# Performance work log

Measured on AMD Instinct MI355X. Metric: run time of the kernel, lower is better.

Reference implementation:

```python
import jax, jax.numpy as jnp
import numpy as np

D_MODEL = 1024
D_HIDDEN = 4096
N_EXPERTS = 8
B, S = 2, 2048


def setup_inputs() -> dict:
    key = jax.random.key(0)
    ks = jax.random.split(key, 4)
    sd = 1.0 / np.sqrt(D_MODEL)
    sh = 1.0 / np.sqrt(D_HIDDEN)
    return {
        "x": jax.random.normal(ks[0], (B, S, D_MODEL), dtype=jnp.float32),
        "Wg": jax.random.normal(ks[1], (D_MODEL, N_EXPERTS), dtype=jnp.float32) * sd,
        "bg": jnp.zeros((N_EXPERTS,), dtype=jnp.float32),
        "W1": jax.random.normal(ks[2], (N_EXPERTS, D_MODEL, D_HIDDEN), dtype=jnp.float32) * sd,
        "b1": jnp.zeros((N_EXPERTS, D_HIDDEN), dtype=jnp.float32),
        "W2": jax.random.normal(ks[3], (N_EXPERTS, D_HIDDEN, D_MODEL), dtype=jnp.float32) * sh,
        "b2": jnp.zeros((N_EXPERTS, D_MODEL), dtype=jnp.float32),
    }


def reference(x, Wg, bg, W1, b1, W2, b2):
    # Router: softmax is monotone, so argmax(softmax(logits)) == argmax(logits).
    logits = jnp.einsum("bsd,de->bse", x, Wg) + bg
    expert_idx = jnp.argmax(logits, axis=-1)  # [B, S]
    # Top-1 dispatch, expressed as compute-all-experts + per-token select
    # (jit-friendly; the torch loop masks/gathers per expert).
    h = jax.nn.gelu(jnp.einsum("bsd,edh->bseh", x, W1) + b1, approximate=False)
    y = jnp.einsum("bseh,ehd->bsed", h, W2) + b2  # [B, S, E, D]
    out = jnp.take_along_axis(y, expert_idx[:, :, None, None], axis=2)[:, :, 0, :]
    return out
```

## Files before the change

kernel.cpp:

```cpp
#include <hip/hip_runtime.h>
#include <hip/hip_bf16.h>
#include <math.h>

#define D_MODEL 1024
#define D_HIDDEN 4096
#define N_EXP 8
#define N_TOK 4096

typedef __attribute__((ext_vector_type(8))) __bf16 bf16x8_t;
typedef __attribute__((ext_vector_type(4))) float f32x4_t;

#define WS_BUCKET_OFF 256
#define WS_XB_OFF     ((size_t)1 << 18)
#define WS_H_OFF      (((size_t)1 << 18) + ((size_t)8 << 20))
#define WS_W1B_OFF    (((size_t)1 << 18) + ((size_t)40 << 20))
#define WS_W2B_OFF    (((size_t)1 << 18) + ((size_t)104 << 20))
#define WS_NEED       (((size_t)1 << 18) + ((size_t)168 << 20))

__device__ __forceinline__ void gload16(const void* g, void* l) {
    __builtin_amdgcn_global_load_lds(
        (__attribute__((address_space(1))) void*)(g),
        (__attribute__((address_space(3))) void*)(l),
        16, 0, 0);
}

template<int N> __device__ __forceinline__ void waitcnt_vm() {
    if constexpr (N >= 8)      asm volatile("s_waitcnt vmcnt(8)" ::: "memory");
    else if constexpr (N == 6) asm volatile("s_waitcnt vmcnt(6)" ::: "memory");
    else if constexpr (N == 4) asm volatile("s_waitcnt vmcnt(4)" ::: "memory");
    else                       asm volatile("s_waitcnt vmcnt(0)" ::: "memory");
}

__global__ __launch_bounds__(64) void init_counts(int* counts) {
    if (threadIdx.x < N_EXP) counts[threadIdx.x] = 0;
}

__global__ __launch_bounds__(256) void router_kernel(
    const float* __restrict__ x, const float* __restrict__ Wg,
    const float* __restrict__ bg, int* __restrict__ counts,
    int* __restrict__ bucket, __hip_bfloat16* __restrict__ xb)
{
    const int wid  = threadIdx.x >> 6;
    const int lane = threadIdx.x & 63;
    const int t    = blockIdx.x * 4 + wid;
    const float* xr = x + (size_t)t * D_MODEL;

    double acc[N_EXP];
#pragma unroll
    for (int e = 0; e < N_EXP; ++e) acc[e] = 0.0;

#pragma unroll
    for (int j = 0; j < D_MODEL / 64; ++j) {
        const int d = j * 64 + lane;
        const float xv = xr[d];
        xb[(size_t)t * D_MODEL + d] = __float2bfloat16(xv);
        const float4* wr = (const float4*)(Wg + (size_t)d * N_EXP);
        const float4 w0 = wr[0], w1 = wr[1];
        const double xd = (double)xv;
        acc[0] += xd * (double)w0.x; acc[1] += xd * (double)w0.y;
        acc[2] += xd * (double)w0.z; acc[3] += xd * (double)w0.w;
        acc[4] += xd * (double)w1.x; acc[5] += xd * (double)w1.y;
        acc[6] += xd * (double)w1.z; acc[7] += xd * (double)w1.w;
    }
#pragma unroll
    for (int e = 0; e < N_EXP; ++e) {
        double v = acc[e];
#pragma unroll
        for (int off = 32; off >= 1; off >>= 1) v += __shfl_xor(v, off, 64);
        acc[e] = v + (double)bg[e];
    }
    if (lane == 0) {
        int best = 0; double bv = acc[0];
#pragma unroll
        for (int e = 1; e < N_EXP; ++e)
            if (acc[e] > bv) { bv = acc[e]; best = e; }
        const int pos = atomicAdd(&counts[best], 1);
        bucket[best * N_TOK + pos] = t;
    }
}

template<int KT, int NT>
__global__ __launch_bounds__(256) void convert_w(
    const float* __restrict__ W, __hip_bfloat16* __restrict__ Wb)
{
    const int e  = blockIdx.z;
    const int k0 = blockIdx.y * 64;
    const int n0 = blockIdx.x * 64;
    const int tid = threadIdx.x;

    __shared__ __hip_bfloat16 Lt[64 * 68];

    const int q  = tid & 15;
    const int kb = tid >> 4;
    const float* src = W + (size_t)e * KT * NT + (size_t)(k0 + kb * 4) * NT + n0 + q * 4;
    float4 v0 = *(const float4*)(src);
    float4 v1 = *(const float4*)(src + (size_t)NT);
    float4 v2 = *(const float4*)(src + (size_t)2 * NT);
    float4 v3 = *(const float4*)(src + (size_t)3 * NT);
#pragma unroll
    for (int i = 0; i < 4; ++i) {
        union { __hip_bfloat16 hh[4]; unsigned long long u; } pk;
        pk.hh[0] = __float2bfloat16(((const float*)&v0)[i]);
        pk.hh[1] = __float2bfloat16(((const float*)&v1)[i]);
        pk.hh[2] = __float2bfloat16(((const float*)&v2)[i]);
        pk.hh[3] = __float2bfloat16(((const float*)&v3)[i]);
        *(unsigned long long*)((char*)Lt + (size_t)(q * 4 + i) * 136 + kb * 8) = pk.u;
    }
    __syncthreads();

    const int w    = tid >> 6;
    const int lane = tid & 63;
    const int nr   = w * 16 + (lane >> 2);
    const int half = lane & 3;
    const char* rp = (const char*)Lt + (size_t)nr * 136 + half * 32;
    const uint2 a0 = *(const uint2*)(rp);
    const uint2 a1 = *(const uint2*)(rp + 8);
    const uint2 b0 = *(const uint2*)(rp + 16);
    const uint2 b1 = *(const uint2*)(rp + 24);
    __hip_bfloat16* op = Wb + (size_t)e * NT * KT + (size_t)(n0 + nr) * KT + k0 + half * 16;
    *(uint4*)op       = make_uint4(a0.x, a0.y, a1.x, a1.y);
    *(uint4*)(op + 8) = make_uint4(b0.x, b0.y, b1.x, b1.y);
}

template<int K_TOT, int N_TOT, int BN, bool IS_FFN1>
__global__ __launch_bounds__(256) void ffn_gemm_bf16(
    const __hip_bfloat16* __restrict__ A,
    const __hip_bfloat16* __restrict__ Wb,
    const float* __restrict__ bias,
    const int* __restrict__ counts,
    const int* __restrict__ bucket,
    __hip_bfloat16* __restrict__ hout,
    float* __restrict__ yout)
{
    constexpr int NG  = BN / 32;
    constexpr int NBI = BN / 32;
    constexpr int NB  = N_TOT / BN;
    constexpr int MB  = N_TOK / 128;
    constexpr int NWG = NB * MB * N_EXP;
    constexpr int ASZ = 128 * 64 * 2;
    constexpr int BSZ = BN * 64 * 2;
    constexpr int NT  = K_TOT / 64;
    constexpr int L   = 4 + NBI;

    const int orig = blockIdx.x;
    const int wg   = (orig & 7) * (NWG >> 3) + (orig >> 3);
    const int e    = wg / (NB * MB);
    const int rem  = wg % (NB * MB);
    const int n0   = (rem / MB) * BN;
    const int m0   = (rem % MB) * 128;

    const int cnt = counts[e];
    if (m0 >= cnt) return;
    const int tid  = threadIdx.x;
    const int lane = tid & 63;
    const int wid  = tid >> 6;
    const int wm   = wid >> 1, wn = wid & 1;

    __shared__ __hip_bfloat16 As[2 * 128 * 64];
    __shared__ __hip_bfloat16 Bs[2 * BN * 64];
    __shared__ int s_tok[128];

    if (tid < 128) {
        int idx = m0 + tid;
        if (idx >= cnt) idx = cnt - 1;
        s_tok[tid] = bucket[e * N_TOK + idx];
    }
    __syncthreads();

    const __hip_bfloat16* gA[4]; char* lA[4];
#pragma unroll
    for (int i = 0; i < 4; ++i) {
        const int r = wid * 32 + i * 8 + (lane >> 3);
        gA[i] = A + (size_t)s_tok[r] * K_TOT + (((lane & 7) ^ (r & 7)) << 3);
        lA[i] = (char*)As + (size_t)(wid * 32 + i * 8) * 128;
    }
    const __hip_bfloat16* gB[NBI]; char* lB[NBI];
    const __hip_bfloat16* wbase = Wb + (size_t)e * N_TOT * K_TOT;
#pragma unroll
    for (int i = 0; i < NBI; ++i) {
        const int r = wid * (BN / 4) + i * 8 + (lane >> 3);
        gB[i] = wbase + (size_t)(n0 + r) * K_TOT + (((lane & 7) ^ (r & 7)) << 3);
        lB[i] = (char*)Bs + (size_t)(wid * (BN / 4) + i * 8) * 128;
    }

    f32x4_t acc[4][NG];
#pragma unroll
    for (int f = 0; f < 4; ++f)
#pragma unroll
        for (int g = 0; g < NG; ++g) acc[f][g] = (f32x4_t){0.f, 0.f, 0.f, 0.f};

#pragma unroll
    for (int i = 0; i < 4; ++i) gload16(gA[i], lA[i]);
#pragma unroll
    for (int i = 0; i < NBI; ++i) gload16(gB[i], lB[i]);
    waitcnt_vm<0>();
    __builtin_amdgcn_s_barrier();

    for (int t = 0; t < NT; ++t) {
        const int c = t & 1;
        if (t + 1 < NT) {
            const int k1 = (t + 1) * 64;
#pragma unroll
            for (int i = 0; i < 4; ++i) gload16(gA[i] + k1, lA[i] + (c ^ 1) * ASZ);
#pragma unroll
            for (int i = 0; i < NBI; ++i) gload16(gB[i] + k1, lB[i] + (c ^ 1) * BSZ);
            waitcnt_vm<L>();
        } else {
            waitcnt_vm<0>();
        }
        __builtin_amdgcn_s_barrier();
        __builtin_amdgcn_sched_barrier(0);

        const char* asb = (const char*)As + c * ASZ;
        const char* bsb = (const char*)Bs + c * BSZ;
#pragma unroll
        for (int kk = 0; kk < 2; ++kk) {
            uint4 af[4], bf[NG];
            const int ko = kk * 4 + (lane >> 4);
#pragma unroll
            for (int f = 0; f < 4; ++f) {
                const int r = wm * 64 + f * 16 + (lane & 15);
                af[f] = *(const uint4*)(asb + r * 128 + ((ko ^ (r & 7)) << 4));
            }
#pragma unroll
            for (int g = 0; g < NG; ++g) {
                const int n = wn * (BN / 2) + g * 16 + (lane & 15);
                bf[g] = *(const uint4*)(bsb + n * 128 + ((ko ^ (n & 7)) << 4));
            }
#pragma unroll
            for (int f = 0; f < 4; ++f)
#pragma unroll
                for (int g = 0; g < NG; ++g)
                    acc[f][g] = __builtin_amdgcn_mfma_f32_16x16x32_bf16(
                        __builtin_bit_cast(bf16x8_t, af[f]),
                        __builtin_bit_cast(bf16x8_t, bf[g]),
                        acc[f][g], 0, 0, 0);
        }
        __builtin_amdgcn_s_barrier();
    }

#pragma unroll
    for (int f = 0; f < 4; ++f) {
#pragma unroll
        for (int j = 0; j < 4; ++j) {
            const int rl = wm * 64 + f * 16 + (lane >> 4) * 4 + j;
            const bool ok = (m0 + rl) < cnt;
            const int tok = s_tok[rl];
#pragma unroll
            for (int g = 0; g < NG; ++g) {
                const int col = n0 + wn * (BN / 2) + g * 16 + (lane & 15);
                float v = acc[f][g][j] + bias[e * N_TOT + col];
                if (IS_FFN1) {
                    v = 0.5f * v * (1.0f + erff(v * 0.70710678118654752f));
                    if (ok) hout[(size_t)tok * N_TOT + col] = __float2bfloat16(v);
                } else {
                    if (ok) yout[(size_t)tok * N_TOT + col] = v;
                }
            }
        }
    }
}

template<int K_TOT, int N_TOT, bool IS_FFN1>
__global__ __launch_bounds__(256, 2) void ffn_gemm_f32(
    const __hip_bfloat16* __restrict__ A,
    const float* __restrict__ W,
    const float* __restrict__ bias,
    const int* __restrict__ counts,
    const int* __restrict__ bucket,
    __hip_bfloat16* __restrict__ hout,
    float* __restrict__ yout)
{
    const int e   = blockIdx.z;
    const int cnt = counts[e];
    const int m0  = blockIdx.y * 128;
    if (m0 >= cnt) return;
    const int n0   = blockIdx.x * 128;
    const int tid  = threadIdx.x;
    const int lane = tid & 63;
    const int wid  = tid >> 6;
    const int wm   = wid >> 1, wn = wid & 1;

    __shared__ __hip_bfloat16 As[128 * 64];
    __shared__ __hip_bfloat16 Bs[128 * 64];
    __shared__ int s_tok[128];

    if (tid < 128) {
        int idx = m0 + tid;
        if (idx >= cnt) idx = cnt - 1;
        s_tok[tid] = bucket[e * N_TOK + idx];
    }
    __syncthreads();

    const __hip_bfloat16* gA[4]; char* lA[4];
#pragma unroll
    for (int i = 0; i < 4; ++i) {
        const int r = wid * 32 + i * 8 + (lane >> 3);
        gA[i] = A + (size_t)s_tok[r] * K_TOT + (((lane & 7) ^ (r & 7)) << 3);
        lA[i] = (char*)As + (size_t)(wid * 32 + i * 8) * 128;
    }
    const int ko_t = lane & 7;
    const int nq   = wid * 8 + (lane >> 3);
    const float* wb = W + (size_t)e * K_TOT * N_TOT + (size_t)(ko_t * 8) * N_TOT + n0 + nq * 4;

    f32x4_t acc[4][4];
#pragma unroll
    for (int f = 0; f < 4; ++f)
#pragma unroll
        for (int g = 0; g < 4; ++g) acc[f][g] = (f32x4_t){0.f, 0.f, 0.f, 0.f};

    for (int k0 = 0; k0 < K_TOT; k0 += 64) {
#pragma unroll
        for (int i = 0; i < 4; ++i) gload16(gA[i] + k0, lA[i]);
        const float* wk = wb + (size_t)k0 * N_TOT;
        float4 v[8];
#pragma unroll
        for (int j = 0; j < 8; ++j) v[j] = *(const float4*)(wk + (size_t)j * N_TOT);
#pragma unroll
        for (int i = 0; i < 4; ++i) {
            const int n = nq * 4 + i;
            union { __hip_bfloat16 hh[8]; uint4 u; } pk;
#pragma unroll
            for (int j = 0; j < 8; ++j) pk.hh[j] = __float2bfloat16(((const float*)&v[j])[i]);
            *(uint4*)((char*)Bs + n * 128 + ((ko_t ^ (n & 7)) << 4)) = pk.u;
        }
        __syncthreads();

#pragma unroll
        for (int kk = 0; kk < 2; ++kk) {
            uint4 af[4], bf[4];
            const int ko = kk * 4 + (lane >> 4);
#pragma unroll
            for (int f = 0; f < 4; ++f) {
                const int r = wm * 64 + f * 16 + (lane & 15);
                af[f] = *(const uint4*)((const char*)As + r * 128 + ((ko ^ (r & 7)) << 4));
            }
#pragma unroll
            for (int g = 0; g < 4; ++g) {
                const int n = wn * 64 + g * 16 + (lane & 15);
                bf[g] = *(const uint4*)((const char*)Bs + n * 128 + ((ko ^ (n & 7)) << 4));
            }
#pragma unroll
            for (int f = 0; f < 4; ++f)
#pragma unroll
                for (int g = 0; g < 4; ++g)
                    acc[f][g] = __builtin_amdgcn_mfma_f32_16x16x32_bf16(
                        __builtin_bit_cast(bf16x8_t, af[f]),
                        __builtin_bit_cast(bf16x8_t, bf[g]),
                        acc[f][g], 0, 0, 0);
        }
        __syncthreads();
    }

#pragma unroll
    for (int f = 0; f < 4; ++f) {
#pragma unroll
        for (int j = 0; j < 4; ++j) {
            const int rl = wm * 64 + f * 16 + (lane >> 4) * 4 + j;
            const bool ok = (m0 + rl) < cnt;
            const int tok = s_tok[rl];
#pragma unroll
            for (int g = 0; g < 4; ++g) {
                const int col = n0 + wn * 64 + g * 16 + (lane & 15);
                float v = acc[f][g][j] + bias[e * N_TOT + col];
                if (IS_FFN1) {
                    v = 0.5f * v * (1.0f + erff(v * 0.70710678118654752f));
                    if (ok) hout[(size_t)tok * N_TOT + col] = __float2bfloat16(v);
                } else {
                    if (ok) yout[(size_t)tok * N_TOT + col] = v;
                }
            }
        }
    }
}

extern "C" void kernel_launch(void* const* d_in, const int* in_sizes, int n_in,
                              void* d_out, int out_size, void* d_ws, size_t ws_size,
                              hipStream_t stream) {
    const float* x  = (const float*)d_in[0];
    const float* Wg = (const float*)d_in[1];
    const float* bg = (const float*)d_in[2];
    const float* W1 = (const float*)d_in[3];
    const float* b1 = (const float*)d_in[4];
    const float* W2 = (const float*)d_in[5];
    const float* b2 = (const float*)d_in[6];
    float* out = (float*)d_out;

    char* ws = (char*)d_ws;
    int* counts = (int*)(ws);
    int* bucket = (int*)(ws + WS_BUCKET_OFF);
    __hip_bfloat16* xb  = (__hip_bfloat16*)(ws + WS_XB_OFF);
    __hip_bfloat16* h   = (__hip_bfloat16*)(ws + WS_H_OFF);
    __hip_bfloat16* w1b = (__hip_bfloat16*)(ws + WS_W1B_OFF);
    __hip_bfloat16* w2b = (__hip_bfloat16*)(ws + WS_W2B_OFF);

    init_counts<<<dim3(1), dim3(64), 0, stream>>>(counts);
    router_kernel<<<dim3(N_TOK / 4), dim3(256), 0, stream>>>(x, Wg, bg, counts, bucket, xb);

    if (ws_size >= WS_NEED) {
        convert_w<D_MODEL, D_HIDDEN><<<dim3(D_HIDDEN / 64, D_MODEL / 64, N_EXP), dim3(256), 0, stream>>>(W1, w1b);
        convert_w<D_HIDDEN, D_MODEL><<<dim3(D_MODEL / 64, D_HIDDEN / 64, N_EXP), dim3(256), 0, stream>>>(W2, w2b);
        ffn_gemm_bf16<D_MODEL, D_HIDDEN, 128, true>
            <<<dim3((D_HIDDEN / 128) * (N_TOK / 128) * N_EXP), dim3(256), 0, stream>>>(
                xb, w1b, b1, counts, bucket, h, nullptr);
        ffn_gemm_bf16<D_HIDDEN, D_MODEL, 64, false>
            <<<dim3((D_MODEL / 64) * (N_TOK / 128) * N_EXP), dim3(256), 0, stream>>>(
                h, w2b, b2, counts, bucket, nullptr, out);
    } else {
        ffn_gemm_f32<D_MODEL, D_HIDDEN, true>
            <<<dim3(D_HIDDEN / 128, N_TOK / 128, N_EXP), dim3(256), 0, stream>>>(
                xb, W1, b1, counts, bucket, h, nullptr);
        ffn_gemm_f32<D_HIDDEN, D_MODEL, false>
            <<<dim3(D_MODEL / 128, N_TOK / 128, N_EXP), dim3(256), 0, stream>>>(
                h, W2, b2, counts, bucket, nullptr, out);
    }
}
```

Baseline: 380.9 us.

## Pre-tile gathered activations and weights into contiguous swizzled chunks for GEMMs

Adds a prefix kernel and a gather kernel that copies each expert's routed tokens into contiguous, pre-swizzled 128x64 bf16 tiles, and rewrites weight conversion to emit the same tiled swizzled layout. The GEMMs then issue fully contiguous global-to-LDS loads with no per-row indirection, and FFN1 writes its hidden output directly in the tiled layout that FFN2 consumes. The aim is to remove scattered row gathers and strided loads from the main loops. In exchange it adds an extra gather pass over x, two more launches and a larger workspace requirement.

```diff
diff --git a/kernel.cpp b/kernel.cpp
--- a/kernel.cpp
+++ b/kernel.cpp
@@ -10,12 +10,15 @@
 typedef __attribute__((ext_vector_type(8))) __bf16 bf16x8_t;
 typedef __attribute__((ext_vector_type(4))) float f32x4_t;
 
+#define WS_PREFIX_OFF 128
 #define WS_BUCKET_OFF 256
 #define WS_XB_OFF     ((size_t)1 << 18)
-#define WS_H_OFF      (((size_t)1 << 18) + ((size_t)8 << 20))
-#define WS_W1B_OFF    (((size_t)1 << 18) + ((size_t)40 << 20))
-#define WS_W2B_OFF    (((size_t)1 << 18) + ((size_t)104 << 20))
-#define WS_NEED       (((size_t)1 << 18) + ((size_t)168 << 20))
+#define WS_HT_OFF     (((size_t)1 << 18) + ((size_t)8 << 20))
+#define WS_W1T_OFF    (((size_t)1 << 18) + ((size_t)50 << 20))
+#define WS_W2T_OFF    (((size_t)1 << 18) + ((size_t)114 << 20))
+#define WS_AE_OFF     (((size_t)1 << 18) + ((size_t)178 << 20))
+#define WS_NEED       (((size_t)1 << 18) + ((size_t)189 << 20))
+#define WS_NEED_FB    (((size_t)1 << 18) + ((size_t)40 << 20))
 
 __device__ __forceinline__ void gload16(const void* g, void* l) {
     __builtin_amdgcn_global_load_lds(
@@ -33,6 +36,14 @@
 
 __global__ __launch_bounds__(64) void init_counts(int* counts) {
     if (threadIdx.x < N_EXP) counts[threadIdx.x] = 0;
+}
+
+__global__ __launch_bounds__(64) void prefix_kernel(const int* counts, int* prefix) {
+    if (threadIdx.x == 0) {
+        int s = 0;
+#pragma unroll
+        for (int e = 0; e < N_EXP; ++e) { prefix[e] = s; s += (counts[e] + 127) >> 7; }
+    }
 }
 
 __global__ __launch_bounds__(256) void router_kernel(
@@ -79,55 +90,110 @@
     }
 }
 
-template<int KT, int NT>
-__global__ __launch_bounds__(256) void convert_w(
-    const float* __restrict__ W, __hip_bfloat16* __restrict__ Wb)
-{
-    const int e  = blockIdx.z;
-    const int k0 = blockIdx.y * 64;
-    const int n0 = blockIdx.x * 64;
+__global__ __launch_bounds__(256) void convert_w1(
+    const float* __restrict__ W, __hip_bfloat16* __restrict__ Wt)
+{
+    const int nblk = blockIdx.x, kc = blockIdx.y, e = blockIdx.z;
+    const int k0 = kc * 64, n0 = nblk * 128;
     const int tid = threadIdx.x;
-
-    __shared__ __hip_bfloat16 Lt[64 * 68];
-
-    const int q  = tid & 15;
-    const int kb = tid >> 4;
-    const float* src = W + (size_t)e * KT * NT + (size_t)(k0 + kb * 4) * NT + n0 + q * 4;
-    float4 v0 = *(const float4*)(src);
-    float4 v1 = *(const float4*)(src + (size_t)NT);
-    float4 v2 = *(const float4*)(src + (size_t)2 * NT);
-    float4 v3 = *(const float4*)(src + (size_t)3 * NT);
-#pragma unroll
-    for (int i = 0; i < 4; ++i) {
-        union { __hip_bfloat16 hh[4]; unsigned long long u; } pk;
-        pk.hh[0] = __float2bfloat16(((const float*)&v0)[i]);
-        pk.hh[1] = __float2bfloat16(((const float*)&v1)[i]);
-        pk.hh[2] = __float2bfloat16(((const float*)&v2)[i]);
-        pk.hh[3] = __float2bfloat16(((const float*)&v3)[i]);
-        *(unsigned long long*)((char*)Lt + (size_t)(q * 4 + i) * 136 + kb * 8) = pk.u;
+    __shared__ __hip_bfloat16 Lt[128 * 72];
+
+    const int kr = tid >> 2;
+    const int cq = tid & 3;
+    const float* src = W + (size_t)e * D_MODEL * D_HIDDEN + (size_t)(k0 + kr) * D_HIDDEN + n0 + cq * 32;
+#pragma unroll
+    for (int f = 0; f < 8; ++f) {
+        const float4 v = *(const float4*)(src + f * 4);
+#pragma unroll
+        for (int j = 0; j < 4; ++j) {
+            const int n = cq * 32 + f * 4 + j;
+            *(__hip_bfloat16*)((char*)Lt + (size_t)n * 144 + kr * 2) = __float2bfloat16(((const float*)&v)[j]);
+        }
     }
     __syncthreads();
 
-    const int w    = tid >> 6;
-    const int lane = tid & 63;
-    const int nr   = w * 16 + (lane >> 2);
-    const int half = lane & 3;
-    const char* rp = (const char*)Lt + (size_t)nr * 136 + half * 32;
-    const uint2 a0 = *(const uint2*)(rp);
-    const uint2 a1 = *(const uint2*)(rp + 8);
-    const uint2 b0 = *(const uint2*)(rp + 16);
-    const uint2 b1 = *(const uint2*)(rp + 24);
-    __hip_bfloat16* op = Wb + (size_t)e * NT * KT + (size_t)(n0 + nr) * KT + k0 + half * 16;
-    *(uint4*)op       = make_uint4(a0.x, a0.y, a1.x, a1.y);
-    *(uint4*)(op + 8) = make_uint4(b0.x, b0.y, b1.x, b1.y);
+    char* outc = (char*)Wt + (((size_t)e * 32 + nblk) * 16 + kc) * 16384;
+    const int n = tid >> 1, half = tid & 1;
+#pragma unroll
+    for (int s = 0; s < 4; ++s) {
+        const int slot = half * 4 + s;
+        const int ko = slot ^ (n & 7);
+        const uint4 v = *(const uint4*)((const char*)Lt + (size_t)n * 144 + ko * 16);
+        *(uint4*)(outc + (size_t)n * 128 + slot * 16) = v;
+    }
+}
+
+__global__ __launch_bounds__(256) void convert_w2(
+    const float* __restrict__ W, __hip_bfloat16* __restrict__ Wt)
+{
+    const int nblk = blockIdx.x, kc = blockIdx.y, e = blockIdx.z;
+    const int k0 = kc * 64, n0 = nblk * 64;
+    const int tid = threadIdx.x;
+    __shared__ __hip_bfloat16 Lt[64 * 72];
+
+    const int kr = tid >> 2;
+    const int cq = tid & 3;
+    const float* src = W + (size_t)e * D_HIDDEN * D_MODEL + (size_t)(k0 + kr) * D_MODEL + n0 + cq * 16;
+#pragma unroll
+    for (int f = 0; f < 4; ++f) {
+        const float4 v = *(const float4*)(src + f * 4);
+#pragma unroll
+        for (int j = 0; j < 4; ++j) {
+            const int n = cq * 16 + f * 4 + j;
+            *(__hip_bfloat16*)((char*)Lt + (size_t)n * 144 + kr * 2) = __float2bfloat16(((const float*)&v)[j]);
+        }
+    }
+    __syncthreads();
+
+    char* outc = (char*)Wt + (((size_t)e * 16 + nblk) * 64 + kc) * 8192;
+    const int n = tid >> 2, q = tid & 3;
+#pragma unroll
+    for (int s = 0; s < 2; ++s) {
+        const int slot = q * 2 + s;
+        const int ko = slot ^ (n & 7);
+        const uint4 v = *(const uint4*)((const char*)Lt + (size_t)n * 144 + ko * 16);
+        *(uint4*)(outc + (size_t)n * 128 + slot * 16) = v;
+    }
+}
+
+__global__ __launch_bounds__(256) void gather_a(
+    const float* __restrict__ x, const int* __restrict__ counts,
+    const int* __restrict__ prefix, const int* __restrict__ bucket,
+    __hip_bfloat16* __restrict__ Ae)
+{
+    const int mblk = blockIdx.x, kc = blockIdx.y, e = blockIdx.z;
+    const int cnt = counts[e];
+    if (mblk * 128 >= cnt) return;
+    const int mbg = prefix[e] + mblk;
+    const int tid = threadIdx.x;
+    const int m = tid >> 1, half = tid & 1;
+    int idx = mblk * 128 + m;
+    if (idx >= cnt) idx = cnt - 1;
+    const int tok = bucket[e * N_TOK + idx];
+    const float* src = x + (size_t)tok * D_MODEL + kc * 64 + half * 32;
+    char* dst = (char*)Ae + ((size_t)mbg * 16 + kc) * 16384 + (size_t)m * 128;
+#pragma unroll
+    for (int s = 0; s < 4; ++s) {
+        const float4 a = *(const float4*)(src + s * 8);
+        const float4 b = *(const float4*)(src + s * 8 + 4);
+        union { __hip_bfloat16 hh[8]; uint4 u; } pk;
+#pragma unroll
+        for (int j = 0; j < 4; ++j) {
+            pk.hh[j]     = __float2bfloat16(((const float*)&a)[j]);
+            pk.hh[j + 4] = __float2bfloat16(((const float*)&b)[j]);
+        }
+        const int ko = half * 4 + s;
+        *(uint4*)(dst + ((ko ^ (m & 7)) << 4)) = pk.u;
+    }
 }
 
 template<int K_TOT, int N_TOT, int BN, bool IS_FFN1>
-__global__ __launch_bounds__(256) void ffn_gemm_bf16(
-    const __hip_bfloat16* __restrict__ A,
-    const __hip_bfloat16* __restrict__ Wb,
+__global__ __launch_bounds__(256) void ffn_gemm_t(
+    const __hip_bfloat16* __restrict__ At,
+    const __hip_bfloat16* __restrict__ Wt,
     const float* __restrict__ bias,
     const int* __restrict__ counts,
+    const int* __restrict__ prefix,
     const int* __restrict__ bucket,
     __hip_bfloat16* __restrict__ hout,
     float* __restrict__ yout)
@@ -137,51 +203,44 @@
     constexpr int NB  = N_TOT / BN;
     constexpr int MB  = N_TOK / 128;
     constexpr int NWG = NB * MB * N_EXP;
-    constexpr int ASZ = 128 * 64 * 2;
-    constexpr int BSZ = BN * 64 * 2;
-    constexpr int NT  = K_TOT / 64;
+    constexpr int KC  = K_TOT / 64;
+    constexpr int ACH = 16384;
+    constexpr int BCH = BN * 128;
+    constexpr int ASZ = 16384;
+    constexpr int BSZ = BN * 128;
     constexpr int L   = 4 + NBI;
 
     const int orig = blockIdx.x;
     const int wg   = (orig & 7) * (NWG >> 3) + (orig >> 3);
     const int e    = wg / (NB * MB);
     const int rem  = wg % (NB * MB);
-    const int n0   = (rem / MB) * BN;
-    const int m0   = (rem % MB) * 128;
-
-    const int cnt = counts[e];
+    const int nblk = rem / MB;
+    const int mblk = rem % MB;
+    const int cnt  = counts[e];
+    const int m0   = mblk * 128;
     if (m0 >= cnt) return;
+    const int mbg  = prefix[e] + mblk;
+    const int n0   = nblk * BN;
+
     const int tid  = threadIdx.x;
     const int lane = tid & 63;
     const int wid  = tid >> 6;
     const int wm   = wid >> 1, wn = wid & 1;
 
-    __shared__ __hip_bfloat16 As[2 * 128 * 64];
-    __shared__ __hip_bfloat16 Bs[2 * BN * 64];
+    __shared__ char As[2 * ASZ];
+    __shared__ char Bs[2 * BSZ];
     __shared__ int s_tok[128];
 
-    if (tid < 128) {
+    if (!IS_FFN1 && tid < 128) {
         int idx = m0 + tid;
         if (idx >= cnt) idx = cnt - 1;
         s_tok[tid] = bucket[e * N_TOK + idx];
     }
-    __syncthreads();
-
-    const __hip_bfloat16* gA[4]; char* lA[4];
-#pragma unroll
-    for (int i = 0; i < 4; ++i) {
-        const int r = wid * 32 + i * 8 + (lane >> 3);
-        gA[i] = A + (size_t)s_tok[r] * K_TOT + (((lane & 7) ^ (r & 7)) << 3);
-        lA[i] = (char*)As + (size_t)(wid * 32 + i * 8) * 128;
-    }
-    const __hip_bfloat16* gB[NBI]; char* lB[NBI];
-    const __hip_bfloat16* wbase = Wb + (size_t)e * N_TOT * K_TOT;
-#pragma unroll
-    for (int i = 0; i < NBI; ++i) {
-        const int r = wid * (BN / 4) + i * 8 + (lane >> 3);
-        gB[i] = wbase + (size_t)(n0 + r) * K_TOT + (((lane & 7) ^ (r & 7)) << 3);
-        lB[i] = (char*)Bs + (size_t)(wid * (BN / 4) + i * 8) * 128;
-    }
+
+    const char* Abase = (const char*)At + (size_t)mbg * KC * ACH;
+    const char* Bbase = (const char*)Wt + ((size_t)e * NB + nblk) * (size_t)KC * BCH;
+    const int aoff = wid * 4096 + lane * 16;
+    const int boff = wid * (BCH / 4) + lane * 16;
 
     f32x4_t acc[4][NG];
 #pragma unroll
@@ -190,20 +249,23 @@
         for (int g = 0; g < NG; ++g) acc[f][g] = (f32x4_t){0.f, 0.f, 0.f, 0.f};
 
 #pragma unroll
-    for (int i = 0; i < 4; ++i) gload16(gA[i], lA[i]);
-#pragma unroll
-    for (int i = 0; i < NBI; ++i) gload16(gB[i], lB[i]);
+    for (int i = 0; i < 4; ++i) gload16(Abase + aoff + i * 1024, As + (aoff - lane * 16) + i * 1024);
+#pragma unroll
+    for (int i = 0; i < NBI; ++i) gload16(Bbase + boff + i * 1024, Bs + (boff - lane * 16) + i * 1024);
     waitcnt_vm<0>();
     __builtin_amdgcn_s_barrier();
 
-    for (int t = 0; t < NT; ++t) {
+    for (int t = 0; t < KC; ++t) {
         const int c = t & 1;
-        if (t + 1 < NT) {
-            const int k1 = (t + 1) * 64;
-#pragma unroll
-            for (int i = 0; i < 4; ++i) gload16(gA[i] + k1, lA[i] + (c ^ 1) * ASZ);
-#pragma unroll
-            for (int i = 0; i < NBI; ++i) gload16(gB[i] + k1, lB[i] + (c ^ 1) * BSZ);
+        if (t + 1 < KC) {
+            const char* An = Abase + (size_t)(t + 1) * ACH;
+            const char* Bn = Bbase + (size_t)(t + 1) * BCH;
+            char* lan = As + (c ^ 1) * ASZ + (aoff - lane * 16);
+            char* lbn = Bs + (c ^ 1) * BSZ + (boff - lane * 16);
+#pragma unroll
+            for (int i = 0; i < 4; ++i) gload16(An + aoff + i * 1024, lan + i * 1024);
+#pragma unroll
+            for (int i = 0; i < NBI; ++i) gload16(Bn + boff + i * 1024, lbn + i * 1024);
             waitcnt_vm<L>();
         } else {
             waitcnt_vm<0>();
@@ -211,8 +273,8 @@
         __builtin_amdgcn_s_barrier();
         __builtin_amdgcn_sched_barrier(0);
 
-        const char* asb = (const char*)As + c * ASZ;
-        const char* bsb = (const char*)Bs + c * BSZ;
+        const char* asb = As + c * ASZ;
+        const char* bsb = Bs + c * BSZ;
 #pragma unroll
         for (int kk = 0; kk < 2; ++kk) {
             uint4 af[4], bf[NG];
@@ -239,21 +301,36 @@
         __builtin_amdgcn_s_barrier();
     }
 
-#pragma unroll
-    for (int f = 0; f < 4; ++f) {
-#pragma unroll
-        for (int j = 0; j < 4; ++j) {
-            const int rl = wm * 64 + f * 16 + (lane >> 4) * 4 + j;
-            const bool ok = (m0 + rl) < cnt;
-            const int tok = s_tok[rl];
-#pragma unroll
-            for (int g = 0; g < NG; ++g) {
-                const int col = n0 + wn * (BN / 2) + g * 16 + (lane & 15);
-                float v = acc[f][g][j] + bias[e * N_TOT + col];
-                if (IS_FFN1) {
+    if (IS_FFN1) {
+        char* hb = (char*)hout + (size_t)mbg * (D_HIDDEN / 64) * 16384;
+#pragma unroll
+        for (int f = 0; f < 4; ++f) {
+#pragma unroll
+            for (int j = 0; j < 4; ++j) {
+                const int m = wm * 64 + f * 16 + (lane >> 4) * 4 + j;
+#pragma unroll
+                for (int g = 0; g < NG; ++g) {
+                    const int col = n0 + wn * (BN / 2) + g * 16 + (lane & 15);
+                    float v = acc[f][g][j] + bias[e * N_TOT + col];
                     v = 0.5f * v * (1.0f + erff(v * 0.70710678118654752f));
-                    if (ok) hout[(size_t)tok * N_TOT + col] = __float2bfloat16(v);
-                } else {
+                    const int kc = col >> 6, kw = col & 63, ko = kw >> 3, b = kw & 7;
+                    *(__hip_bfloat16*)(hb + ((size_t)kc * 128 + m) * 128 +
+                                       (((ko ^ (m & 7)) << 4) + (b << 1))) = __float2bfloat16(v);
+                }
+            }
+        }
+    } else {
+#pragma unroll
+        for (int f = 0; f < 4; ++f) {
+#pragma unroll
+            for (int j = 0; j < 4; ++j) {
+                const int rl = wm * 64 + f * 16 + (lane >> 4) * 4 + j;
+                const bool ok = (m0 + rl) < cnt;
+                const int tok = s_tok[rl];
+#pragma unroll
+                for (int g = 0; g < NG; ++g) {
+                    const int col = n0 + wn * (BN / 2) + g * 16 + (lane & 15);
+                    const float v = acc[f][g][j] + bias[e * N_TOT + col];
                     if (ok) yout[(size_t)tok * N_TOT + col] = v;
                 }
             }
@@ -388,25 +465,30 @@
 
     char* ws = (char*)d_ws;
     int* counts = (int*)(ws);
+    int* prefix = (int*)(ws + WS_PREFIX_OFF);
     int* bucket = (int*)(ws + WS_BUCKET_OFF);
     __hip_bfloat16* xb  = (__hip_bfloat16*)(ws + WS_XB_OFF);
-    __hip_bfloat16* h   = (__hip_bfloat16*)(ws + WS_H_OFF);
-    __hip_bfloat16* w1b = (__hip_bfloat16*)(ws + WS_W1B_OFF);
-    __hip_bfloat16* w2b = (__hip_bfloat16*)(ws + WS_W2B_OFF);
+    __hip_bfloat16* ht  = (__hip_bfloat16*)(ws + WS_HT_OFF);
+    __hip_bfloat16* w1t = (__hip_bfloat16*)(ws + WS_W1T_OFF);
+    __hip_bfloat16* w2t = (__hip_bfloat16*)(ws + WS_W2T_OFF);
+    __hip_bfloat16* ae  = (__hip_bfloat16*)(ws + WS_AE_OFF);
 
     init_counts<<<dim3(1), dim3(64), 0, stream>>>(counts);
     router_kernel<<<dim3(N_TOK / 4), dim3(256), 0, stream>>>(x, Wg, bg, counts, bucket, xb);
+    prefix_kernel<<<dim3(1), dim3(64), 0, stream>>>(counts, prefix);
 
     if (ws_size >= WS_NEED) {
-        convert_w<D_MODEL, D_HIDDEN><<<dim3(D_HIDDEN / 64, D_MODEL / 64, N_EXP), dim3(256), 0, stream>>>(W1, w1b);
-        convert_w<D_HIDDEN, D_MODEL><<<dim3(D_MODEL / 64, D_HIDDEN / 64, N_EXP), dim3(256), 0, stream>>>(W2, w2b);
-        ffn_gemm_bf16<D_MODEL, D_HIDDEN, 128, true>
+        convert_w1<<<dim3(32, 16, N_EXP), dim3(256), 0, stream>>>(W1, w1t);
+        convert_w2<<<dim3(16, 64, N_EXP), dim3(256), 0, stream>>>(W2, w2t);
+        gather_a<<<dim3(32, 16, N_EXP), dim3(256), 0, stream>>>(x, counts, prefix, bucket, ae);
+        ffn_gemm_t<D_MODEL, D_HIDDEN, 128, true>
             <<<dim3((D_HIDDEN / 128) * (N_TOK / 128) * N_EXP), dim3(256), 0, stream>>>(
-                xb, w1b, b1, counts, bucket, h, nullptr);
-        ffn_gemm_bf16<D_HIDDEN, D_MODEL, 64, false>
+                ae, w1t, b1, counts, prefix, bucket, ht, nullptr);
+        ffn_gemm_t<D_HIDDEN, D_MODEL, 64, false>
             <<<dim3((D_MODEL / 64) * (N_TOK / 128) * N_EXP), dim3(256), 0, stream>>>(
-                h, w2b, b2, counts, bucket, nullptr, out);
+                ht, w2t, b2, counts, prefix, bucket, nullptr, out);
     } else {
+        __hip_bfloat16* h = ht;
         ffn_gemm_f32<D_MODEL, D_HIDDEN, true>
             <<<dim3(D_HIDDEN / 128, N_TOK / 128, N_EXP), dim3(256), 0, stream>>>(
                 xb, W1, b1, counts, bucket, h, nullptr);
```

After: 434.3 us. +14.0%, slower.
